# Kernel optimization log

Hardware: AMD Instinct MI355X
Metric: run time of the kernel (lower is better)

## Reference

```python
import jax, jax.numpy as jnp
import numpy as np

D = 64      # n_embd (== head_size in this module)
H = 8       # n_heads
B = 4
T = 2048    # seq len == block_size
EPS = 1e-5


def layernorm(x, g, b):
    mu = jnp.mean(x, axis=-1, keepdims=True)
    var = jnp.mean(jnp.square(x - mu), axis=-1, keepdims=True)
    return (x - mu) * jax.lax.rsqrt(var + EPS) * g + b


def setup_inputs() -> dict:
    key = jax.random.key(0)
    ks = jax.random.split(key, 16)
    s = 1.0 / np.sqrt(D)
    inp = {
        'inputs': jax.random.normal(ks[0], (B, T, D), jnp.float32),
        # per-head QKV linears: weight [H, D, D] (in, out), bias [H, D]
        'Wq': jax.random.uniform(ks[1], (H, D, D), jnp.float32, -s, s),
        'bq': jax.random.uniform(ks[2], (H, D), jnp.float32, -s, s),
        'Wk': jax.random.uniform(ks[3], (H, D, D), jnp.float32, -s, s),
        'bk': jax.random.uniform(ks[4], (H, D), jnp.float32, -s, s),
        'Wv': jax.random.uniform(ks[5], (H, D, D), jnp.float32, -s, s),
        'bv': jax.random.uniform(ks[6], (H, D), jnp.float32, -s, s),
        # projection: Linear(H*D -> D)
        'Wp': jax.random.uniform(ks[7], (H * D, D), jnp.float32, -1/np.sqrt(H*D), 1/np.sqrt(H*D)),
        'bp': jax.random.uniform(ks[8], (D,), jnp.float32, -1/np.sqrt(H*D), 1/np.sqrt(H*D)),
        # FFN: D -> 4D -> D
        'W1': jax.random.uniform(ks[9], (D, 4 * D), jnp.float32, -s, s),
        'b1': jax.random.uniform(ks[10], (4 * D,), jnp.float32, -s, s),
        'W2': jax.random.uniform(ks[11], (4 * D, D), jnp.float32, -1/np.sqrt(4*D), 1/np.sqrt(4*D)),
        'b2': jax.random.uniform(ks[12], (D,), jnp.float32, -1/np.sqrt(4*D), 1/np.sqrt(4*D)),
        'g1': jnp.ones((D,), jnp.float32), 'be1': jnp.zeros((D,), jnp.float32),
        'g2': jnp.ones((D,), jnp.float32), 'be2': jnp.zeros((D,), jnp.float32),
    }
    return inp


def reference(inputs, Wq, bq, Wk, bk, Wv, bv, Wp, bp, W1, b1, W2, b2, g1, be1, g2, be2):
    x = inputs
    # per-head full-width QKV: [H, B, T, D]
    q = jnp.einsum('btd,hde->hbte', x, Wq) + bq[:, None, None, :]
    k = jnp.einsum('btd,hde->hbte', x, Wk) + bk[:, None, None, :]
    v = jnp.einsum('btd,hde->hbte', x, Wv) + bv[:, None, None, :]
    # unscaled scores (module has no 1/sqrt(d) scaling)
    scores = jnp.einsum('hbte,hbse->hbts', q, k)  # [H, B, T, T]
    causal = jnp.tril(jnp.ones((T, T), bool))
    scores = jnp.where(causal, scores, -jnp.inf)
    attn = jax.nn.softmax(scores, axis=-1)
    out = jnp.einsum('hbts,hbse->hbte', attn, v)  # [H, B, T, D]
    # torch.cat over heads along last dim -> [B, T, H*D]
    cat = jnp.transpose(out, (1, 2, 0, 3)).reshape(B, T, H * D)
    attn_out = cat @ Wp + bp
    h1 = layernorm(x + attn_out, g1, be1)
    ffn = jax.nn.relu(h1 @ W1 + b1) @ W2 + b2
    return layernorm(h1 + ffn, g2, be2)
```

## Files before the change

kernel.cpp:

```cpp
#include <hip/hip_runtime.h>
#include <hip/hip_bf16.h>
#include <stdint.h>

#define Dd 64
#define Hh 8
#define Bb 4
#define Tt 2048
#define NT (Bb * Tt)

typedef __attribute__((ext_vector_type(4))) float f32x4;
typedef __attribute__((ext_vector_type(8))) __bf16 bf16x8;
typedef __attribute__((ext_vector_type(8))) uint16_t u16x8;
typedef __attribute__((ext_vector_type(4))) uint16_t u16x4;

__device__ __forceinline__ uint16_t f2bf_fast(float f) {
    union { __bf16 h; uint16_t u; } c; c.h = (__bf16)f; return c.u;
}
__device__ __forceinline__ uint32_t pkbf(float a, float b) {
    return (uint32_t)f2bf_fast(a) | ((uint32_t)f2bf_fast(b) << 16);
}

#define SWZ(row, k)   ((row) * 72  + ((k) ^ ((((row) >> 3) & 7) << 3)))
#define PSZ(q, k)     ((q)  * 72  + ((k) ^ ((((q)  >> 2) & 3) << 3)))
#define HSZ(q, k)     ((q)  * 264 + ((k) ^ ((((q)  >> 2) & 3) << 3)))
#define W2SWZ(col, k) ((col) * 264 + ((k) ^ ((((col) >> 3) & 7) << 3)))
#define WPSWZ(col, k) ((col) * 520 + ((k) ^ ((((col) >> 3) & 7) << 3)))

#define LOG2E 1.44269504f

__global__ __launch_bounds__(256) void setup_kernel(
    const float* __restrict__ x,
    const float* __restrict__ Wq, const float* __restrict__ Wk,
    const float* __restrict__ Wv, const float* __restrict__ Wp,
    const float* __restrict__ W1, const float* __restrict__ W2,
    uint16_t* __restrict__ xb, uint16_t* __restrict__ WtAll,
    uint16_t* __restrict__ WptS, uint16_t* __restrict__ W1g,
    uint16_t* __restrict__ W2g)
{
    const int bid = blockIdx.x, t = threadIdx.x;
    if (bid < 256) {
        size_t base = ((size_t)bid * 256 + t) * 8;
        f32x4 a = *(const f32x4*)&x[base];
        f32x4 b = *(const f32x4*)&x[base + 4];
        u16x8 o;
#pragma unroll
        for (int j = 0; j < 4; ++j) { o[j] = f2bf_fast(a[j]); o[4 + j] = f2bf_fast(b[j]); }
        *(u16x8*)&xb[base] = o;
    } else if (bid < 280) {
        const int mh = bid - 256, m = mh / 8, h = mh % 8;
        const float* W = (m == 0) ? Wq : (m == 1) ? Wk : Wv;
        uint16_t* dst = WtAll + (size_t)mh * 4608;
#pragma unroll
        for (int p = 0; p < 4; ++p) {
            int idx = p * 256 + t;
            int k = idx >> 4, c4 = (idx & 15) * 4;
            f32x4 wv = *(const f32x4*)&W[(size_t)(h * 64 + k) * 64 + c4];
#pragma unroll
            for (int j = 0; j < 4; ++j) dst[SWZ(c4 + j, k)] = f2bf_fast(wv[j]);
        }
    } else if (bid < 288) {
        const int j = bid - 280;
#pragma unroll
        for (int p = 0; p < 16; ++p) {
            int idx = p * 256 + t;
            int col = idx & 63, k = j * 64 + (idx >> 6);
            WptS[WPSWZ(col, k)] = f2bf_fast(Wp[(size_t)k * 64 + col]);
        }
    } else if (bid < 292) {
        const int j = bid - 288;
#pragma unroll
        for (int p = 0; p < 16; ++p) {
            int e = j * 4096 + p * 256 + t;
            int col = e & 255, k = e >> 8;
            W1g[SWZ(col, k)] = f2bf_fast(W1[(size_t)k * 256 + col]);
        }
    } else {
        const int j = bid - 292;
#pragma unroll
        for (int p = 0; p < 16; ++p) {
            int e = j * 4096 + p * 256 + t;
            int col = e & 63, k = e >> 6;
            W2g[W2SWZ(col, k)] = f2bf_fast(W2[(size_t)k * 64 + col]);
        }
    }
}

__global__ __launch_bounds__(256) void qkv_kernel(
    const uint16_t* __restrict__ xb, const uint16_t* __restrict__ WtAll,
    const float* __restrict__ bq, const float* __restrict__ bk,
    const float* __restrict__ bv,
    uint16_t* __restrict__ qb, uint16_t* __restrict__ kb, uint16_t* __restrict__ vb)
{
    __shared__ uint16_t WtF[3][64 * 72];
    const int rt = blockIdx.x, h = blockIdx.y;
    const int t = threadIdx.x, lane = t & 63, w = t >> 6;
    const int l15 = lane & 15, g = lane >> 4;

#pragma unroll
    for (int m = 0; m < 3; ++m) {
        const u16x8* src = (const u16x8*)(WtAll + (size_t)(m * 8 + h) * 4608);
        u16x8* dst = (u16x8*)WtF[m];
        dst[t] = src[t];
        dst[256 + t] = src[256 + t];
        if (t < 64) dst[512 + t] = src[512 + t];
    }
    const int row = rt * 64 + w * 16 + l15;
    bf16x8 a0 = *(const bf16x8*)&xb[(size_t)row * 64 + g * 8];
    bf16x8 a1 = *(const bf16x8*)&xb[(size_t)row * 64 + 32 + g * 8];
    __syncthreads();

#pragma unroll
    for (int m = 0; m < 3; ++m) {
        const float* bias = (m == 0) ? bq : (m == 1) ? bk : bv;
        f32x4 acc[4] = {};
#pragma unroll
        for (int ct = 0; ct < 4; ++ct) {
            bf16x8 b0 = *(const bf16x8*)&WtF[m][SWZ(ct * 16 + l15, g * 8)];
            bf16x8 b1 = *(const bf16x8*)&WtF[m][SWZ(ct * 16 + l15, 32 + g * 8)];
            acc[ct] = __builtin_amdgcn_mfma_f32_16x16x32_bf16(a0, b0, acc[ct], 0, 0, 0);
            acc[ct] = __builtin_amdgcn_mfma_f32_16x16x32_bf16(a1, b1, acc[ct], 0, 0, 0);
        }
        if (m < 2) {
            uint16_t* out = (m == 0) ? qb : kb;
            const float scl = (m == 0) ? LOG2E : 1.0f;
#pragma unroll
            for (int ct = 0; ct < 4; ++ct) {
                float bb = bias[h * 64 + ct * 16 + l15];
#pragma unroll
                for (int rr = 0; rr < 4; ++rr) {
                    int orow = rt * 64 + w * 16 + g * 4 + rr;
                    out[((size_t)h * NT + orow) * 64 + ct * 16 + l15] =
                        f2bf_fast((acc[ct][rr] + bb) * scl);
                }
            }
        } else {
            const size_t tb = ((size_t)h * NT + (size_t)rt * 64) * 64;
            const int kcol = (w >> 1) * 32 + g * 8 + (w & 1) * 4;
#pragma unroll
            for (int ct = 0; ct < 4; ++ct) {
                float bb = bias[h * 64 + ct * 16 + l15];
                u16x4 vo;
#pragma unroll
                for (int rr = 0; rr < 4; ++rr) vo[rr] = f2bf_fast(acc[ct][rr] + bb);
                *(u16x4*)&vb[tb + (size_t)(ct * 16 + l15) * 64 + kcol] = vo;
            }
        }
    }
}

__global__ __launch_bounds__(256) void attn_kernel8(
    const uint16_t* __restrict__ qb, const uint16_t* __restrict__ kb,
    const uint16_t* __restrict__ vb, uint16_t* __restrict__ cat)
{
    __shared__ uint16_t KsF[2][64 * 72];
    __shared__ uint16_t VtF[2][64 * 72];
    const int bid = blockIdx.x;
    const int lbid = (bid & 7) * 64 + (bid >> 3);
    const int pairid = lbid & 15;
    const int hb = lbid >> 4;
    const int h = hb & 7, b = hb >> 3;
    const int t = threadIdx.x, lane = t & 63, w = t >> 6;
    const int l15 = lane & 15, g = lane >> 4;
    const size_t base = ((size_t)h * NT + (size_t)b * Tt) * 64;
    const uint16_t* Qh  = qb + base;
    const uint16_t* Kh  = kb + base;
    const uint16_t* VhT = vb + base;

    union { uint32_t u[4]; bf16x8 v; } onesu;
#pragma unroll
    for (int j = 0; j < 4; ++j) onesu.u[j] = 0x3F803F80u;
    const bf16x8 ones = onesu.v;

    for (int ph = 0; ph < 2; ++ph) {
        const int qt = ph ? (31 - pairid) : pairid;
        bf16x8 aq0, aq1;
        {
            int qrow = qt * 64 + w * 16 + l15;
            aq0 = *(const bf16x8*)&Qh[(size_t)qrow * 64 + g * 8];
            aq1 = *(const bf16x8*)&Qh[(size_t)qrow * 64 + 32 + g * 8];
        }
        f32x4 o[4] = {};
        f32x4 l_acc = {};
        float m_run = -INFINITY;

        __syncthreads();
#pragma unroll
        for (int i = 0; i < 2; ++i) {
            int slot = i * 256 + t;
            int r = slot >> 3, c8 = (slot & 7) * 8;
            size_t off = (size_t)r * 64 + c8;
            u16x8 kk = *(const u16x8*)&Kh[off];
            u16x8 vv = *(const u16x8*)&VhT[off];
            *(u16x8*)&KsF[0][SWZ(r, c8)] = kk;
            *(u16x8*)&VtF[0][SWZ(r, c8)] = vv;
        }
        __syncthreads();

        const int nkv = qt + 1;
        for (int kv = 0; kv < nkv; ++kv) {
            const int cur = kv & 1;
            const bool pf = (kv + 1) < nkv;
            u16x8 pK[2], pV[2];
            if (pf) {
                const size_t poff = (size_t)(kv + 1) * 4096;
#pragma unroll
                for (int i = 0; i < 2; ++i) {
                    int slot = i * 256 + t;
                    size_t off = poff + (size_t)(slot >> 3) * 64 + (slot & 7) * 8;
                    pK[i] = *(const u16x8*)&Kh[off];
                    pV[i] = *(const u16x8*)&VhT[off];
                }
            }
            f32x4 s[4];
#pragma unroll
            for (int kt = 0; kt < 4; ++kt) {
                bf16x8 bk0 = *(const bf16x8*)&KsF[cur][SWZ(kt * 16 + l15, g * 8)];
                bf16x8 bk1 = *(const bf16x8*)&KsF[cur][SWZ(kt * 16 + l15, 32 + g * 8)];
                f32x4 z = {};
                z = __builtin_amdgcn_mfma_f32_16x16x32_bf16(bk0, aq0, z, 0, 0, 0);
                z = __builtin_amdgcn_mfma_f32_16x16x32_bf16(bk1, aq1, z, 0, 0, 0);
                s[kt] = z;
            }
            if (kv == nkv - 1) {
                int qlocal = w * 16 + l15;
#pragma unroll
                for (int kt = 0; kt < 4; ++kt)
#pragma unroll
                    for (int rj = 0; rj < 4; ++rj)
                        if (kt * 16 + g * 4 + rj > qlocal) s[kt][rj] = -INFINITY;
            }
            float mt = fmaxf(fmaxf(fmaxf(s[0][0], s[0][1]), fmaxf(s[0][2], s[0][3])),
                             fmaxf(fmaxf(s[1][0], s[1][1]), fmaxf(s[1][2], s[1][3])));
            mt = fmaxf(mt, fmaxf(fmaxf(fmaxf(s[2][0], s[2][1]), fmaxf(s[2][2], s[2][3])),
                                 fmaxf(fmaxf(s[3][0], s[3][1]), fmaxf(s[3][2], s[3][3]))));
            mt = fmaxf(mt, __shfl_xor(mt, 16));
            mt = fmaxf(mt, __shfl_xor(mt, 32));
            if (__any((int)(mt > m_run + 11.5409f))) {
                float mnew = fmaxf(m_run, mt);
                float alpha = exp2f(m_run - mnew);
                m_run = mnew;
                float a0 = __shfl(alpha, g * 4 + 0);
                float a1 = __shfl(alpha, g * 4 + 1);
                float a2 = __shfl(alpha, g * 4 + 2);
                float a3 = __shfl(alpha, g * 4 + 3);
                l_acc[0] *= a0; l_acc[1] *= a1; l_acc[2] *= a2; l_acc[3] *= a3;
#pragma unroll
                for (int dt = 0; dt < 4; ++dt) {
                    o[dt][0] *= a0; o[dt][1] *= a1; o[dt][2] *= a2; o[dt][3] *= a3;
                }
            }
#pragma unroll
            for (int kt = 0; kt < 4; ++kt)
#pragma unroll
                for (int rj = 0; rj < 4; ++rj)
                    s[kt][rj] = exp2f(s[kt][rj] - m_run);
            union { uint32_t wd[4]; bf16x8 v; } ap0, ap1;
            ap0.wd[0] = pkbf(s[0][0], s[0][1]); ap0.wd[1] = pkbf(s[0][2], s[0][3]);
            ap0.wd[2] = pkbf(s[1][0], s[1][1]); ap0.wd[3] = pkbf(s[1][2], s[1][3]);
            ap1.wd[0] = pkbf(s[2][0], s[2][1]); ap1.wd[1] = pkbf(s[2][2], s[2][3]);
            ap1.wd[2] = pkbf(s[3][0], s[3][1]); ap1.wd[3] = pkbf(s[3][2], s[3][3]);
#pragma unroll
            for (int c = 0; c < 2; ++c) {
                const bf16x8 ap = c ? ap1.v : ap0.v;
                l_acc = __builtin_amdgcn_mfma_f32_16x16x32_bf16(ap, ones, l_acc, 0, 0, 0);
#pragma unroll
                for (int dt = 0; dt < 4; ++dt) {
                    bf16x8 bv = *(const bf16x8*)&VtF[cur][SWZ(dt * 16 + l15, c * 32 + g * 8)];
                    o[dt] = __builtin_amdgcn_mfma_f32_16x16x32_bf16(ap, bv, o[dt], 0, 0, 0);
                }
            }
            if (pf) {
#pragma unroll
                for (int i = 0; i < 2; ++i) {
                    int slot = i * 256 + t;
                    int r = slot >> 3, c8 = (slot & 7) * 8;
                    *(u16x8*)&KsF[cur ^ 1][SWZ(r, c8)] = pK[i];
                    *(u16x8*)&VtF[cur ^ 1][SWZ(r, c8)] = pV[i];
                }
                __syncthreads();
            }
        }
        f32x4 inv;
#pragma unroll
        for (int rj = 0; rj < 4; ++rj) inv[rj] = 1.f / l_acc[rj];
#pragma unroll
        for (int dt = 0; dt < 4; ++dt) {
            int rowb = qt * 64 + w * 16 + g * 4;
            size_t cb = ((size_t)b * Tt + rowb) * 512 + h * 64 + dt * 16 + l15;
            cat[cb]        = f2bf_fast(o[dt][0] * inv[0]);
            cat[cb + 512]  = f2bf_fast(o[dt][1] * inv[1]);
            cat[cb + 1024] = f2bf_fast(o[dt][2] * inv[2]);
            cat[cb + 1536] = f2bf_fast(o[dt][3] * inv[3]);
        }
    }
}

__global__ __launch_bounds__(128) void tail_kernel(
    const uint16_t* __restrict__ cat, const uint16_t* __restrict__ WptS,
    const uint16_t* __restrict__ W1g, const uint16_t* __restrict__ W2g,
    const float* __restrict__ bp, const float* __restrict__ b1,
    const float* __restrict__ b2, const float* __restrict__ x,
    const float* __restrict__ g1, const float* __restrict__ be1,
    const float* __restrict__ g2, const float* __restrict__ be2,
    float* __restrict__ out)
{
    __shared__ uint16_t h1S[2][16 * 72];
    __shared__ uint16_t hidS[2][16 * 264];
    const int rt = blockIdx.x;
    const int t = threadIdx.x, lane = t & 63, w = t >> 6;
    const int l15 = lane & 15, g = lane >> 4;
    const int arow = rt * 32 + w * 16 + l15;

    f32x4 acc[4] = {};
#pragma unroll
    for (int kt = 0; kt < 16; ++kt) {
        bf16x8 a = *(const bf16x8*)&cat[(size_t)arow * 512 + kt * 32 + g * 8];
#pragma unroll
        for (int ct = 0; ct < 4; ++ct) {
            bf16x8 bfr = *(const bf16x8*)&WptS[WPSWZ(ct * 16 + l15, kt * 32 + g * 8)];
            acc[ct] = __builtin_amdgcn_mfma_f32_16x16x32_bf16(a, bfr, acc[ct], 0, 0, 0);
        }
    }
    float bpv[4], g1v[4], b1v[4];
#pragma unroll
    for (int ct = 0; ct < 4; ++ct) {
        bpv[ct] = bp[ct * 16 + l15];
        g1v[ct] = g1[ct * 16 + l15];
        b1v[ct] = be1[ct * 16 + l15];
    }
    float hv[4][4];
#pragma unroll
    for (int rr = 0; rr < 4; ++rr) {
        int drow = rt * 32 + w * 16 + g * 4 + rr;
        float s[4], sum = 0.f;
#pragma unroll
        for (int ct = 0; ct < 4; ++ct) {
            s[ct] = acc[ct][rr] + bpv[ct] + x[(size_t)drow * 64 + ct * 16 + l15];
            sum += s[ct];
        }
        sum += __shfl_xor(sum, 1); sum += __shfl_xor(sum, 2);
        sum += __shfl_xor(sum, 4); sum += __shfl_xor(sum, 8);
        float mu = sum * (1.f / 64.f);
        float v = 0.f;
#pragma unroll
        for (int ct = 0; ct < 4; ++ct) { s[ct] -= mu; v += s[ct] * s[ct]; }
        v += __shfl_xor(v, 1); v += __shfl_xor(v, 2);
        v += __shfl_xor(v, 4); v += __shfl_xor(v, 8);
        float rstd = rsqrtf(v * (1.f / 64.f) + 1e-5f);
#pragma unroll
        for (int ct = 0; ct < 4; ++ct) {
            float h = s[ct] * rstd * g1v[ct] + b1v[ct];
            hv[ct][rr] = h;
            h1S[w][PSZ(g * 4 + rr, ct * 16 + l15)] = f2bf_fast(h);
        }
    }
    bf16x8 ha0 = *(const bf16x8*)&h1S[w][PSZ(l15, g * 8)];
    bf16x8 ha1 = *(const bf16x8*)&h1S[w][PSZ(l15, 32 + g * 8)];
#pragma unroll
    for (int nt = 0; nt < 16; ++nt) {
        f32x4 a1c = {};
        bf16x8 w10 = *(const bf16x8*)&W1g[SWZ(nt * 16 + l15, g * 8)];
        bf16x8 w11 = *(const bf16x8*)&W1g[SWZ(nt * 16 + l15, 32 + g * 8)];
        a1c = __builtin_amdgcn_mfma_f32_16x16x32_bf16(ha0, w10, a1c, 0, 0, 0);
        a1c = __builtin_amdgcn_mfma_f32_16x16x32_bf16(ha1, w11, a1c, 0, 0, 0);
        float bb1 = b1[nt * 16 + l15];
#pragma unroll
        for (int rr = 0; rr < 4; ++rr)
            hidS[w][HSZ(g * 4 + rr, nt * 16 + l15)] =
                f2bf_fast(fmaxf(a1c[rr] + bb1, 0.f));
    }
    f32x4 acc2[4] = {};
#pragma unroll
    for (int ks = 0; ks < 8; ++ks) {
        bf16x8 hfr = *(const bf16x8*)&hidS[w][HSZ(l15, ks * 32 + g * 8)];
#pragma unroll
        for (int ct = 0; ct < 4; ++ct) {
            bf16x8 w2f = *(const bf16x8*)&W2g[W2SWZ(ct * 16 + l15, ks * 32 + g * 8)];
            acc2[ct] = __builtin_amdgcn_mfma_f32_16x16x32_bf16(hfr, w2f, acc2[ct], 0, 0, 0);
        }
    }
    float b2v[4], g2v[4], be2v[4];
#pragma unroll
    for (int ct = 0; ct < 4; ++ct) {
        b2v[ct]  = b2[ct * 16 + l15];
        g2v[ct]  = g2[ct * 16 + l15];
        be2v[ct] = be2[ct * 16 + l15];
    }
#pragma unroll
    for (int rr = 0; rr < 4; ++rr) {
        int drow = rt * 32 + w * 16 + g * 4 + rr;
        float s[4], sum = 0.f;
#pragma unroll
        for (int ct = 0; ct < 4; ++ct) {
            s[ct] = acc2[ct][rr] + b2v[ct] + hv[ct][rr];
            sum += s[ct];
        }
        sum += __shfl_xor(sum, 1); sum += __shfl_xor(sum, 2);
        sum += __shfl_xor(sum, 4); sum += __shfl_xor(sum, 8);
        float mu = sum * (1.f / 64.f);
        float v = 0.f;
#pragma unroll
        for (int ct = 0; ct < 4; ++ct) { s[ct] -= mu; v += s[ct] * s[ct]; }
        v += __shfl_xor(v, 1); v += __shfl_xor(v, 2);
        v += __shfl_xor(v, 4); v += __shfl_xor(v, 8);
        float rstd = rsqrtf(v * (1.f / 64.f) + 1e-5f);
#pragma unroll
        for (int ct = 0; ct < 4; ++ct)
            out[(size_t)drow * 64 + ct * 16 + l15] =
                s[ct] * rstd * g2v[ct] + be2v[ct];
    }
}

extern "C" void kernel_launch(void* const* d_in, const int* in_sizes, int n_in,
                              void* d_out, int out_size, void* d_ws, size_t ws_size,
                              hipStream_t stream)
{
    (void)in_sizes; (void)n_in; (void)out_size; (void)ws_size;
    const float* x   = (const float*)d_in[0];
    const float* Wq  = (const float*)d_in[1];
    const float* bq  = (const float*)d_in[2];
    const float* Wk  = (const float*)d_in[3];
    const float* bk  = (const float*)d_in[4];
    const float* Wv  = (const float*)d_in[5];
    const float* bv  = (const float*)d_in[6];
    const float* Wp  = (const float*)d_in[7];
    const float* bp  = (const float*)d_in[8];
    const float* W1  = (const float*)d_in[9];
    const float* b1  = (const float*)d_in[10];
    const float* W2  = (const float*)d_in[11];
    const float* b2  = (const float*)d_in[12];
    const float* g1  = (const float*)d_in[13];
    const float* be1 = (const float*)d_in[14];
    const float* g2  = (const float*)d_in[15];
    const float* be2 = (const float*)d_in[16];
    float* outp = (float*)d_out;

    char* w = (char*)d_ws;
    uint16_t* qb   = (uint16_t*)w;
    uint16_t* kb   = qb + (size_t)Hh * NT * 64;
    uint16_t* vb   = kb + (size_t)Hh * NT * 64;
    uint16_t* cat  = vb + (size_t)Hh * NT * 64;
    uint16_t* WptS = cat + (size_t)NT * 512;
    uint16_t* W1g  = WptS + 33280;
    uint16_t* W2g  = W1g + 18432;
    uint16_t* xb   = W2g + 16896;
    uint16_t* WtAll= xb + (size_t)NT * 64;

    setup_kernel<<<dim3(296), dim3(256), 0, stream>>>(
        x, Wq, Wk, Wv, Wp, W1, W2, xb, WtAll, WptS, W1g, W2g);
    qkv_kernel<<<dim3(NT / 64, Hh), dim3(256), 0, stream>>>(
        xb, WtAll, bq, bk, bv, qb, kb, vb);
    attn_kernel8<<<dim3(512), dim3(256), 0, stream>>>(qb, kb, vb, cat);
    tail_kernel<<<dim3(256), dim3(128), 0, stream>>>(
        cat, WptS, W1g, W2g, bp, b1, b2, x, g1, be1, g2, be2, outp);
}
```

Baseline: 162.6 us.

## Use 128-row query tiles with 8 waves sharing each KV tile instead of paired tiles

The attention kernel now gives each block one 128-row query tile handled by 8 waves (512 threads), so every K/V tile staged in shared memory serves twice as many query rows. This replaces the earlier scheme where each block ran two 64-row tiles in sequence, paired for causal load balance. Blocks are issued heaviest-first (qt = 15 - index) so that larger-work blocks start earlier. The cost is uneven per-block work now that pairing is gone, plus a causal mask applied over the last two KV tiles, some of which is wasted on fully masked tiles.

Measured after the change: 188.3 us. 15.8% more time.

```diff
diff --git a/kernel.cpp b/kernel.cpp
--- a/kernel.cpp
+++ b/kernel.cpp
@@ -148,7 +148,7 @@
     }
 }
 
-__global__ __launch_bounds__(256) void attn_kernel8(
+__global__ __launch_bounds__(512) void attn_kernel9(
     const uint16_t* __restrict__ qb, const uint16_t* __restrict__ kb,
     const uint16_t* __restrict__ vb, uint16_t* __restrict__ cat)
 {
@@ -156,7 +156,7 @@
     __shared__ uint16_t VtF[2][64 * 72];
     const int bid = blockIdx.x;
     const int lbid = (bid & 7) * 64 + (bid >> 3);
-    const int pairid = lbid & 15;
+    const int qt = 15 - (lbid & 15);
     const int hb = lbid >> 4;
     const int h = hb & 7, b = hb >> 3;
     const int t = threadIdx.x, lane = t & 63, w = t >> 6;
@@ -171,127 +171,113 @@
     for (int j = 0; j < 4; ++j) onesu.u[j] = 0x3F803F80u;
     const bf16x8 ones = onesu.v;
 
-    for (int ph = 0; ph < 2; ++ph) {
-        const int qt = ph ? (31 - pairid) : pairid;
-        bf16x8 aq0, aq1;
-        {
-            int qrow = qt * 64 + w * 16 + l15;
-            aq0 = *(const bf16x8*)&Qh[(size_t)qrow * 64 + g * 8];
-            aq1 = *(const bf16x8*)&Qh[(size_t)qrow * 64 + 32 + g * 8];
-        }
-        f32x4 o[4] = {};
-        f32x4 l_acc = {};
-        float m_run = -INFINITY;
-
-        __syncthreads();
-#pragma unroll
-        for (int i = 0; i < 2; ++i) {
-            int slot = i * 256 + t;
-            int r = slot >> 3, c8 = (slot & 7) * 8;
-            size_t off = (size_t)r * 64 + c8;
-            u16x8 kk = *(const u16x8*)&Kh[off];
-            u16x8 vv = *(const u16x8*)&VhT[off];
-            *(u16x8*)&KsF[0][SWZ(r, c8)] = kk;
-            *(u16x8*)&VtF[0][SWZ(r, c8)] = vv;
-        }
-        __syncthreads();
-
-        const int nkv = qt + 1;
-        for (int kv = 0; kv < nkv; ++kv) {
-            const int cur = kv & 1;
-            const bool pf = (kv + 1) < nkv;
-            u16x8 pK[2], pV[2];
-            if (pf) {
-                const size_t poff = (size_t)(kv + 1) * 4096;
-#pragma unroll
-                for (int i = 0; i < 2; ++i) {
-                    int slot = i * 256 + t;
-                    size_t off = poff + (size_t)(slot >> 3) * 64 + (slot & 7) * 8;
-                    pK[i] = *(const u16x8*)&Kh[off];
-                    pV[i] = *(const u16x8*)&VhT[off];
-                }
+    const int qlocal = w * 16 + l15;
+    bf16x8 aq0, aq1;
+    {
+        int qrow = qt * 128 + qlocal;
+        aq0 = *(const bf16x8*)&Qh[(size_t)qrow * 64 + g * 8];
+        aq1 = *(const bf16x8*)&Qh[(size_t)qrow * 64 + 32 + g * 8];
+    }
+    f32x4 o[4] = {};
+    f32x4 l_acc = {};
+    float m_run = -INFINITY;
+
+    {
+        int r = t >> 3, c8 = (t & 7) * 8;
+        size_t off = (size_t)r * 64 + c8;
+        u16x8 kk = *(const u16x8*)&Kh[off];
+        u16x8 vv = *(const u16x8*)&VhT[off];
+        *(u16x8*)&KsF[0][SWZ(r, c8)] = kk;
+        *(u16x8*)&VtF[0][SWZ(r, c8)] = vv;
+    }
+    __syncthreads();
+
+    const int nkv = 2 * qt + 2;
+    for (int kv = 0; kv < nkv; ++kv) {
+        const int cur = kv & 1;
+        const bool pf = (kv + 1) < nkv;
+        u16x8 pK, pV;
+        if (pf) {
+            size_t off = (size_t)(kv + 1) * 4096 + (size_t)(t >> 3) * 64 + (t & 7) * 8;
+            pK = *(const u16x8*)&Kh[off];
+            pV = *(const u16x8*)&VhT[off];
+        }
+        f32x4 s[4];
+#pragma unroll
+        for (int kt = 0; kt < 4; ++kt) {
+            bf16x8 bk0 = *(const bf16x8*)&KsF[cur][SWZ(kt * 16 + l15, g * 8)];
+            bf16x8 bk1 = *(const bf16x8*)&KsF[cur][SWZ(kt * 16 + l15, 32 + g * 8)];
+            f32x4 z = {};
+            z = __builtin_amdgcn_mfma_f32_16x16x32_bf16(bk0, aq0, z, 0, 0, 0);
+            z = __builtin_amdgcn_mfma_f32_16x16x32_bf16(bk1, aq1, z, 0, 0, 0);
+            s[kt] = z;
+        }
+        if (kv >= 2 * qt) {
+            const int koff = (kv - 2 * qt) * 64;
+#pragma unroll
+            for (int kt = 0; kt < 4; ++kt)
+#pragma unroll
+                for (int rj = 0; rj < 4; ++rj)
+                    if (koff + kt * 16 + g * 4 + rj > qlocal) s[kt][rj] = -INFINITY;
+        }
+        float mt = fmaxf(fmaxf(fmaxf(s[0][0], s[0][1]), fmaxf(s[0][2], s[0][3])),
+                         fmaxf(fmaxf(s[1][0], s[1][1]), fmaxf(s[1][2], s[1][3])));
+        mt = fmaxf(mt, fmaxf(fmaxf(fmaxf(s[2][0], s[2][1]), fmaxf(s[2][2], s[2][3])),
+                             fmaxf(fmaxf(s[3][0], s[3][1]), fmaxf(s[3][2], s[3][3]))));
+        mt = fmaxf(mt, __shfl_xor(mt, 16));
+        mt = fmaxf(mt, __shfl_xor(mt, 32));
+        if (__any((int)(mt > m_run + 11.5409f))) {
+            float mnew = fmaxf(m_run, mt);
+            float alpha = exp2f(m_run - mnew);
+            m_run = mnew;
+            float a0 = __shfl(alpha, g * 4 + 0);
+            float a1 = __shfl(alpha, g * 4 + 1);
+            float a2 = __shfl(alpha, g * 4 + 2);
+            float a3 = __shfl(alpha, g * 4 + 3);
+            l_acc[0] *= a0; l_acc[1] *= a1; l_acc[2] *= a2; l_acc[3] *= a3;
+#pragma unroll
+            for (int dt = 0; dt < 4; ++dt) {
+                o[dt][0] *= a0; o[dt][1] *= a1; o[dt][2] *= a2; o[dt][3] *= a3;
             }
-            f32x4 s[4];
-#pragma unroll
-            for (int kt = 0; kt < 4; ++kt) {
-                bf16x8 bk0 = *(const bf16x8*)&KsF[cur][SWZ(kt * 16 + l15, g * 8)];
-                bf16x8 bk1 = *(const bf16x8*)&KsF[cur][SWZ(kt * 16 + l15, 32 + g * 8)];
-                f32x4 z = {};
-                z = __builtin_amdgcn_mfma_f32_16x16x32_bf16(bk0, aq0, z, 0, 0, 0);
-                z = __builtin_amdgcn_mfma_f32_16x16x32_bf16(bk1, aq1, z, 0, 0, 0);
-                s[kt] = z;
+        }
+#pragma unroll
+        for (int kt = 0; kt < 4; ++kt)
+#pragma unroll
+            for (int rj = 0; rj < 4; ++rj)
+                s[kt][rj] = exp2f(s[kt][rj] - m_run);
+        union { uint32_t wd[4]; bf16x8 v; } ap0, ap1;
+        ap0.wd[0] = pkbf(s[0][0], s[0][1]); ap0.wd[1] = pkbf(s[0][2], s[0][3]);
+        ap0.wd[2] = pkbf(s[1][0], s[1][1]); ap0.wd[3] = pkbf(s[1][2], s[1][3]);
+        ap1.wd[0] = pkbf(s[2][0], s[2][1]); ap1.wd[1] = pkbf(s[2][2], s[2][3]);
+        ap1.wd[2] = pkbf(s[3][0], s[3][1]); ap1.wd[3] = pkbf(s[3][2], s[3][3]);
+#pragma unroll
+        for (int c = 0; c < 2; ++c) {
+            const bf16x8 ap = c ? ap1.v : ap0.v;
+            l_acc = __builtin_amdgcn_mfma_f32_16x16x32_bf16(ap, ones, l_acc, 0, 0, 0);
+#pragma unroll
+            for (int dt = 0; dt < 4; ++dt) {
+                bf16x8 bv = *(const bf16x8*)&VtF[cur][SWZ(dt * 16 + l15, c * 32 + g * 8)];
+                o[dt] = __builtin_amdgcn_mfma_f32_16x16x32_bf16(ap, bv, o[dt], 0, 0, 0);
             }
-            if (kv == nkv - 1) {
-                int qlocal = w * 16 + l15;
-#pragma unroll
-                for (int kt = 0; kt < 4; ++kt)
-#pragma unroll
-                    for (int rj = 0; rj < 4; ++rj)
-                        if (kt * 16 + g * 4 + rj > qlocal) s[kt][rj] = -INFINITY;
-            }
-            float mt = fmaxf(fmaxf(fmaxf(s[0][0], s[0][1]), fmaxf(s[0][2], s[0][3])),
-                             fmaxf(fmaxf(s[1][0], s[1][1]), fmaxf(s[1][2], s[1][3])));
-            mt = fmaxf(mt, fmaxf(fmaxf(fmaxf(s[2][0], s[2][1]), fmaxf(s[2][2], s[2][3])),
-                                 fmaxf(fmaxf(s[3][0], s[3][1]), fmaxf(s[3][2], s[3][3]))));
-            mt = fmaxf(mt, __shfl_xor(mt, 16));
-            mt = fmaxf(mt, __shfl_xor(mt, 32));
-            if (__any((int)(mt > m_run + 11.5409f))) {
-                float mnew = fmaxf(m_run, mt);
-                float alpha = exp2f(m_run - mnew);
-                m_run = mnew;
-                float a0 = __shfl(alpha, g * 4 + 0);
-                float a1 = __shfl(alpha, g * 4 + 1);
-                float a2 = __shfl(alpha, g * 4 + 2);
-                float a3 = __shfl(alpha, g * 4 + 3);
-                l_acc[0] *= a0; l_acc[1] *= a1; l_acc[2] *= a2; l_acc[3] *= a3;
-#pragma unroll
-                for (int dt = 0; dt < 4; ++dt) {
-                    o[dt][0] *= a0; o[dt][1] *= a1; o[dt][2] *= a2; o[dt][3] *= a3;
-                }
-            }
-#pragma unroll
-            for (int kt = 0; kt < 4; ++kt)
-#pragma unroll
-                for (int rj = 0; rj < 4; ++rj)
-                    s[kt][rj] = exp2f(s[kt][rj] - m_run);
-            union { uint32_t wd[4]; bf16x8 v; } ap0, ap1;
-            ap0.wd[0] = pkbf(s[0][0], s[0][1]); ap0.wd[1] = pkbf(s[0][2], s[0][3]);
-            ap0.wd[2] = pkbf(s[1][0], s[1][1]); ap0.wd[3] = pkbf(s[1][2], s[1][3]);
-            ap1.wd[0] = pkbf(s[2][0], s[2][1]); ap1.wd[1] = pkbf(s[2][2], s[2][3]);
-            ap1.wd[2] = pkbf(s[3][0], s[3][1]); ap1.wd[3] = pkbf(s[3][2], s[3][3]);
-#pragma unroll
-            for (int c = 0; c < 2; ++c) {
-                const bf16x8 ap = c ? ap1.v : ap0.v;
-                l_acc = __builtin_amdgcn_mfma_f32_16x16x32_bf16(ap, ones, l_acc, 0, 0, 0);
-#pragma unroll
-                for (int dt = 0; dt < 4; ++dt) {
-                    bf16x8 bv = *(const bf16x8*)&VtF[cur][SWZ(dt * 16 + l15, c * 32 + g * 8)];
-                    o[dt] = __builtin_amdgcn_mfma_f32_16x16x32_bf16(ap, bv, o[dt], 0, 0, 0);
-                }
-            }
-            if (pf) {
-#pragma unroll
-                for (int i = 0; i < 2; ++i) {
-                    int slot = i * 256 + t;
-                    int r = slot >> 3, c8 = (slot & 7) * 8;
-                    *(u16x8*)&KsF[cur ^ 1][SWZ(r, c8)] = pK[i];
-                    *(u16x8*)&VtF[cur ^ 1][SWZ(r, c8)] = pV[i];
-                }
-                __syncthreads();
-            }
-        }
-        f32x4 inv;
-#pragma unroll
-        for (int rj = 0; rj < 4; ++rj) inv[rj] = 1.f / l_acc[rj];
-#pragma unroll
-        for (int dt = 0; dt < 4; ++dt) {
-            int rowb = qt * 64 + w * 16 + g * 4;
-            size_t cb = ((size_t)b * Tt + rowb) * 512 + h * 64 + dt * 16 + l15;
-            cat[cb]        = f2bf_fast(o[dt][0] * inv[0]);
-            cat[cb + 512]  = f2bf_fast(o[dt][1] * inv[1]);
-            cat[cb + 1024] = f2bf_fast(o[dt][2] * inv[2]);
-            cat[cb + 1536] = f2bf_fast(o[dt][3] * inv[3]);
-        }
+        }
+        if (pf) {
+            int r = t >> 3, c8 = (t & 7) * 8;
+            *(u16x8*)&KsF[cur ^ 1][SWZ(r, c8)] = pK;
+            *(u16x8*)&VtF[cur ^ 1][SWZ(r, c8)] = pV;
+            __syncthreads();
+        }
+    }
+    f32x4 inv;
+#pragma unroll
+    for (int rj = 0; rj < 4; ++rj) inv[rj] = 1.f / l_acc[rj];
+#pragma unroll
+    for (int dt = 0; dt < 4; ++dt) {
+        int rowb = qt * 128 + w * 16 + g * 4;
+        size_t cb = ((size_t)b * Tt + rowb) * 512 + h * 64 + dt * 16 + l15;
+        cat[cb]        = f2bf_fast(o[dt][0] * inv[0]);
+        cat[cb + 512]  = f2bf_fast(o[dt][1] * inv[1]);
+        cat[cb + 1024] = f2bf_fast(o[dt][2] * inv[2]);
+        cat[cb + 1536] = f2bf_fast(o[dt][3] * inv[3]);
     }
 }
 
@@ -450,7 +436,7 @@
         x, Wq, Wk, Wv, Wp, W1, W2, xb, WtAll, WptS, W1g, W2g);
     qkv_kernel<<<dim3(NT / 64, Hh), dim3(256), 0, stream>>>(
         xb, WtAll, bq, bk, bv, qb, kb, vb);
-    attn_kernel8<<<dim3(512), dim3(256), 0, stream>>>(qb, kb, vb, cat);
+    attn_kernel9<<<dim3(512), dim3(512), 0, stream>>>(qb, kb, vb, cat);
     tail_kernel<<<dim3(256), dim3(128), 0, stream>>>(
         cat, WptS, W1g, W2g, bp, b1, b2, x, g1, be1, g2, be2, outp);
 }
```
